# Kernel tuning notes

Measured on AMD Instinct MI355X. Metric: run time of the kernel, lower is better.

The kernel has to match this reference:

```python
import jax, jax.numpy as jnp
import numpy as np

B, S, D_IN, D = 2, 4096, 1024, 64  # batch, seq_len, input_dim, head dim d


def setup_inputs() -> dict:
    key = jax.random.key(0)
    k1, k2, k3, k4 = jax.random.split(key, 4)
    X = jax.random.normal(k1, (B, S, D_IN), dtype=jnp.float32)
    W_q = jax.random.normal(k2, (D_IN, 2 * D), dtype=jnp.float32) / np.sqrt(D_IN)
    W_k = jax.random.normal(k3, (D_IN, 2 * D), dtype=jnp.float32) / np.sqrt(D_IN)
    W_v = jax.random.normal(k4, (D_IN, 2 * D), dtype=jnp.float32) / np.sqrt(D_IN)
    lam = jnp.float32(0.8)
    return {"X": X, "W_q": W_q, "W_k": W_k, "W_v": W_v, "lam": lam}


def reference(X, W_q, W_k, W_v, lam):
    d = W_q.shape[-1] // 2
    Q = X @ W_q  # [B, S, 2d]
    K = X @ W_k  # [B, S, 2d]
    V = X @ W_v  # [B, S, 2d]
    Q1, Q2 = Q[..., :d], Q[..., d:]
    K1, K2 = K[..., :d], K[..., d:]
    s = 1.0 / jnp.sqrt(jnp.float32(d))
    A1 = jnp.einsum("bqd,bkd->bqk", Q1, K1) * s  # [B, S, S]
    A2 = jnp.einsum("bqd,bkd->bqk", Q2, K2) * s  # [B, S, S]
    P = jax.nn.softmax(A1, axis=-1) - lam * jax.nn.softmax(A2, axis=-1)
    return jnp.einsum("bqk,bkv->bqv", P, V)  # [B, S, 2d]
```

## Files before the change

kernel.cpp:

```cpp
#include <hip/hip_runtime.h>
#include <hip/hip_bf16.h>

typedef float f32x4 __attribute__((ext_vector_type(4)));
typedef float f32x16 __attribute__((ext_vector_type(16)));
typedef short bf16x8 __attribute__((ext_vector_type(8)));

#define MFMA16(A,B,C) __builtin_amdgcn_mfma_f32_16x16x32_bf16(A,B,C,0,0,0)
#define MFMA32(A,B,C) __builtin_amdgcn_mfma_f32_32x32x16_bf16(A,B,C,0,0,0)

__device__ __forceinline__ unsigned short f2bf(float f) {
    union { float f; unsigned u; } x; x.f = f;
    return (unsigned short)((x.u + 0x7FFFu + ((x.u >> 16) & 1u)) >> 16);
}

__device__ __forceinline__ float bf2f(unsigned short u) {
    union { unsigned u; float f; } x; x.u = ((unsigned)u) << 16; return x.f;
}

__device__ __forceinline__ unsigned fbits(float f) {
    union { float f; unsigned u; } x; x.f = f; return x.u;
}

__device__ __forceinline__ f32x16 zero16() {
    f32x16 z;
#pragma unroll
    for (int i = 0; i < 16; ++i) z[i] = 0.f;
    return z;
}

typedef const __attribute__((address_space(1))) unsigned int* as1_t;
typedef __attribute__((address_space(3))) unsigned int* as3_t;
__device__ __forceinline__ void gl_lds16(const unsigned short* g, unsigned short* l) {
    __builtin_amdgcn_global_load_lds((as1_t)g, (as3_t)l, 16, 0, 0);
}

__global__ void prep_wt(const float* __restrict__ Wq, const float* __restrict__ Wk,
                        const float* __restrict__ Wv, unsigned short* __restrict__ WT) {
    int w = blockIdx.x % 3;
    int kt = blockIdx.x / 3;
    const float* src = (w == 0) ? Wq : (w == 1) ? Wk : Wv;
    int k0 = kt * 32;
#pragma unroll
    for (int j = 0; j < 16; ++j) {
        int idx = threadIdx.x + j * 256;
        int r = idx >> 7, c = idx & 127;
        float v = src[(size_t)(k0 + r) * 128 + c];
        WT[(size_t)(w * 128 + c) * 1024 + k0 + r] = f2bf(v);
    }
}

__global__ __launch_bounds__(256) void prep_x(const float* __restrict__ X,
                                              unsigned short* __restrict__ Xb) {
    int i = blockIdx.x * 256 + threadIdx.x;
#pragma unroll
    for (int r = 0; r < 8; ++r) {
        int idx = i + r * 262144;
        float4 x = ((const float4*)X)[idx];
        ushort4 p;
        p.x = f2bf(x.x); p.y = f2bf(x.y); p.z = f2bf(x.z); p.w = f2bf(x.w);
        ((ushort4*)Xb)[idx] = p;
    }
}

__global__ __launch_bounds__(256) void proj(const unsigned short* __restrict__ Xb,
        const unsigned short* __restrict__ WT, unsigned short* __restrict__ Qc,
        unsigned short* __restrict__ Kc, unsigned short* __restrict__ VT) {
    int tid = threadIdx.x;
    int w = tid >> 6, lane = tid & 63;
    int lr = lane & 15, lg = lane >> 4;
    int wr = w >> 1, wc = w & 1;
    int m0 = blockIdx.x * 64;
    int n0 = blockIdx.y * 96;

    __shared__ __align__(16) unsigned short Ab[3][64 * 64];
    __shared__ __align__(16) unsigned short Bb[3][96 * 64];

    f32x4 acc[2][3];
#pragma unroll
    for (int i = 0; i < 2; ++i)
#pragma unroll
        for (int j = 0; j < 3; ++j) acc[i][j] = f32x4{0.f,0.f,0.f,0.f};

    int srow = lane >> 3;
    int sunit = lane & 7;
    const unsigned short* aSrc = Xb + (size_t)(m0 + srow) * 1024 + sunit * 8;
    const unsigned short* bSrc = WT + (size_t)(n0 + srow) * 1024 + sunit * 8;

    auto STAGE = [&](unsigned short* ad, unsigned short* bd, int st) {
        int kk = st * 64;
#pragma unroll
        for (int i = 0; i < 2; ++i) {
            int blk = w * 2 + i;
            gl_lds16(aSrc + (size_t)blk * 8 * 1024 + kk, ad + blk * 512);
        }
#pragma unroll
        for (int i = 0; i < 3; ++i) {
            int blk = w * 3 + i;
            gl_lds16(bSrc + (size_t)blk * 8 * 1024 + kk, bd + blk * 512);
        }
    };

    unsigned short *a0 = Ab[0], *a1 = Ab[1], *a2 = Ab[2];
    unsigned short *b0 = Bb[0], *b1 = Bb[1], *b2 = Bb[2];
    STAGE(a0, b0, 0);
    STAGE(a1, b1, 1);

    for (int st = 0; st < 16; ++st) {
        if (st < 15) asm volatile("s_waitcnt vmcnt(5)" ::: "memory");
        else         asm volatile("s_waitcnt vmcnt(0)" ::: "memory");
        __builtin_amdgcn_sched_barrier(0);
        __builtin_amdgcn_s_barrier();
        __builtin_amdgcn_sched_barrier(0);
        if (st + 2 < 16) STAGE(a2, b2, st + 2);

        const unsigned short* ab = a0;
        const unsigned short* bb = b0;
#pragma unroll
        for (int ksub = 0; ksub < 2; ++ksub) {
            int ko = ksub * 32 + lg * 8;
            bf16x8 af[2], bf[3];
#pragma unroll
            for (int mt = 0; mt < 2; ++mt)
                af[mt] = *(const bf16x8*)(ab + (wr * 32 + mt * 16 + lr) * 64 + ko);
#pragma unroll
            for (int nt = 0; nt < 3; ++nt)
                bf[nt] = *(const bf16x8*)(bb + (wc * 48 + nt * 16 + lr) * 64 + ko);
#pragma unroll
            for (int mt = 0; mt < 2; ++mt)
#pragma unroll
                for (int nt = 0; nt < 3; ++nt)
                    acc[mt][nt] = MFMA16(af[mt], bf[nt], acc[mt][nt]);
        }
        unsigned short* t;
        t = a0; a0 = a1; a1 = a2; a2 = t;
        t = b0; b0 = b1; b1 = b2; b2 = t;
    }

    int b = m0 >> 12;
    int sbase = (m0 & 4095) + wr * 32;
#pragma unroll
    for (int nt = 0; nt < 3; ++nt) {
        int gcol = n0 + wc * 48 + nt * 16 + lr;
        int tensor = gcol >> 7;
#pragma unroll
        for (int mt = 0; mt < 2; ++mt) {
            int sloc = sbase + mt * 16 + 4 * lg;
            if (tensor == 2) {
                int vcol = gcol & 127;
                int slocV = (sloc & ~15) | (((lg & 1) << 3) | ((lg >> 1) << 2));
                ushort4 pk;
                pk.x = f2bf(acc[mt][nt][0]); pk.y = f2bf(acc[mt][nt][1]);
                pk.z = f2bf(acc[mt][nt][2]); pk.w = f2bf(acc[mt][nt][3]);
                *(ushort4*)(VT + (size_t)(b * 128 + vcol) * 4096 + slocV) = pk;
            } else {
                int within = gcol & 127;
                int comp = within >> 6;
                int col64 = within & 63;
                float sc = (tensor == 0) ? 0.1803368801f : 1.0f;
                unsigned short* dst = (tensor == 0) ? Qc : Kc;
                size_t rowb = (size_t)(comp * 2 + b) * 4096 + sloc;
#pragma unroll
                for (int r = 0; r < 4; ++r)
                    dst[(rowb + r) * 64 + col64] = f2bf(acc[mt][nt][r] * sc);
            }
        }
    }
}

__global__ __launch_bounds__(256, 2) void attn(const unsigned short* __restrict__ Qc,
        const unsigned short* __restrict__ Kc, const unsigned short* __restrict__ VT,
        unsigned short* __restrict__ Opart, float* __restrict__ Lpart) {
    int tid = threadIdx.x;
    int wave = tid >> 6, lane = tid & 63;
    int l31 = lane & 31, hi = lane >> 5;
    int x7 = l31 & 7;
    int b = blockIdx.y;
    int comp = blockIdx.z >> 2, split = blockIdx.z & 3;
    int q0 = blockIdx.x * 128 + wave * 32;
    int kstart = split * 1024;

    __shared__ __align__(16) unsigned short kb3[3][64 * 64];
    __shared__ __align__(16) unsigned short vb3[3][128 * 64];

    const unsigned short* Qp = Qc + ((size_t)(comp * 2 + b) * 4096 + q0 + l31) * 64 + hi * 8;
    bf16x8 qB0 = *(const bf16x8*)(Qp);
    bf16x8 qB1 = *(const bf16x8*)(Qp + 16);
    bf16x8 qB2 = *(const bf16x8*)(Qp + 32);
    bf16x8 qB3 = *(const bf16x8*)(Qp + 48);

    f32x16 o[4];
#pragma unroll
    for (int i = 0; i < 4; ++i) o[i] = zero16();
    f32x16 ol = zero16();
    bf16x8 ones;
#pragma unroll
    for (int i = 0; i < 8; ++i) ones[i] = (short)0x3F80;

    const unsigned short* kSrc = Kc + ((size_t)(comp * 2 + b) * 4096 + kstart
                                       + wave * 8 + (lane >> 3)) * 64
                                    + ((lane & 7) ^ (lane >> 3)) * 8;
    const unsigned short* vSrc = VT + ((size_t)b * 128 + (tid >> 3)) * 4096
                                    + kstart + ((lane & 7) ^ (lane >> 3)) * 8;

    auto STAGE = [&](unsigned short* kd, unsigned short* vd, int it) {
        const unsigned short* ks = kSrc + (size_t)it * 4096;
        gl_lds16(ks,        kd + wave * 512);
        gl_lds16(ks + 2048, kd + 2048 + wave * 512);
        const unsigned short* vs = vSrc + it * 64;
#pragma unroll
        for (int ri = 0; ri < 4; ++ri)
            gl_lds16(vs + (size_t)ri * 32 * 4096, vd + ri * 2048 + wave * 512);
    };

    unsigned short *k0 = kb3[0], *k1 = kb3[1], *k2 = kb3[2];
    unsigned short *v0 = vb3[0], *v1 = vb3[1], *v2 = vb3[2];
    STAGE(k0, v0, 0);
    STAGE(k1, v1, 1);

    for (int it = 0; it < 16; ++it) {
        if (it < 15) asm volatile("s_waitcnt vmcnt(6)" ::: "memory");
        else         asm volatile("s_waitcnt vmcnt(0)" ::: "memory");
        __builtin_amdgcn_sched_barrier(0);
        __builtin_amdgcn_s_barrier();
        __builtin_amdgcn_sched_barrier(0);
        if (it + 2 < 16) STAGE(k2, v2, it + 2);

        const unsigned short* kb = k0;
        const unsigned short* vb = v0;

        f32x16 st0 = zero16(), st1 = zero16();
        __builtin_amdgcn_s_setprio(1);
#pragma unroll
        for (int j = 0; j < 4; ++j) {
            int ku = ((j * 2 + hi) ^ x7) * 8;
            bf16x8 kA0 = *(const bf16x8*)(kb + l31 * 64 + ku);
            bf16x8 kA1 = *(const bf16x8*)(kb + (32 + l31) * 64 + ku);
            bf16x8 qj = (j == 0) ? qB0 : (j == 1) ? qB1 : (j == 2) ? qB2 : qB3;
            st0 = MFMA32(kA0, qj, st0);
            st1 = MFMA32(kA1, qj, st1);
        }
        __builtin_amdgcn_s_setprio(0);

        union W4 { unsigned u[4]; bf16x8 v; };
        W4 wA0, wB0, wA1, wB1;
#pragma unroll
        for (int i2 = 0; i2 < 4; ++i2) {
            float a0 = __builtin_amdgcn_exp2f(st0[2 * i2]);
            float a1 = __builtin_amdgcn_exp2f(st0[2 * i2 + 1]);
            float a2 = __builtin_amdgcn_exp2f(st0[8 + 2 * i2]);
            float a3 = __builtin_amdgcn_exp2f(st0[9 + 2 * i2]);
            float b0 = __builtin_amdgcn_exp2f(st1[2 * i2]);
            float b1 = __builtin_amdgcn_exp2f(st1[2 * i2 + 1]);
            float b2 = __builtin_amdgcn_exp2f(st1[8 + 2 * i2]);
            float b3 = __builtin_amdgcn_exp2f(st1[9 + 2 * i2]);
            wA0.u[i2] = __builtin_amdgcn_perm(fbits(a1), fbits(a0), 0x07060302);
            wB0.u[i2] = __builtin_amdgcn_perm(fbits(a3), fbits(a2), 0x07060302);
            wA1.u[i2] = __builtin_amdgcn_perm(fbits(b1), fbits(b0), 0x07060302);
            wB1.u[i2] = __builtin_amdgcn_perm(fbits(b3), fbits(b2), 0x07060302);
        }

        __builtin_amdgcn_s_setprio(1);
        ol = MFMA32(wA0.v, ones, ol);
        ol = MFMA32(wB0.v, ones, ol);
        ol = MFMA32(wA1.v, ones, ol);
        ol = MFMA32(wB1.v, ones, ol);
#pragma unroll
        for (int vt = 0; vt < 4; ++vt) {
            const unsigned short* vrow = vb + (vt * 32 + l31) * 64;
            o[vt] = MFMA32(wA0.v, *(const bf16x8*)(vrow + ((0 + hi) ^ x7) * 8), o[vt]);
            o[vt] = MFMA32(wB0.v, *(const bf16x8*)(vrow + ((2 + hi) ^ x7) * 8), o[vt]);
            o[vt] = MFMA32(wA1.v, *(const bf16x8*)(vrow + ((4 + hi) ^ x7) * 8), o[vt]);
            o[vt] = MFMA32(wB1.v, *(const bf16x8*)(vrow + ((6 + hi) ^ x7) * 8), o[vt]);
        }
        __builtin_amdgcn_s_setprio(0);

        unsigned short* t;
        t = k0; k0 = k1; k1 = k2; k2 = t;
        t = v0; v0 = v1; v1 = v2; v2 = t;
    }

    int base = (b * 2 + comp) * 4 + split;
    unsigned short* op = Opart + (size_t)base * 4096 * 128;
#pragma unroll
    for (int vt = 0; vt < 4; ++vt)
#pragma unroll
        for (int r = 0; r < 16; ++r) {
            int qr = (r & 3) + 8 * (r >> 2) + 4 * hi;
            op[(size_t)(q0 + qr) * 128 + vt * 32 + l31] = f2bf(o[vt][r]);
        }
    if (l31 == 0) {
        float* lp = Lpart + (size_t)base * 4096 + q0;
#pragma unroll
        for (int r = 0; r < 16; ++r)
            lp[(r & 3) + 8 * (r >> 2) + 4 * hi] = ol[r];
    }
}

__global__ __launch_bounds__(256) void combine(const unsigned short* __restrict__ Opart,
        const float* __restrict__ Lpart, const float* __restrict__ lamp,
        float* __restrict__ out) {
    float lam = lamp[0];
    int i = blockIdx.x * 256 + threadIdx.x;
    int row = i >> 5;
    int c4  = i & 31;
    int b = row >> 12, q = row & 4095;

    float l1 = 0.f, l2 = 0.f;
#pragma unroll
    for (int s = 0; s < 4; ++s) {
        l1 += Lpart[((size_t)((b * 2 + 0) * 4 + s)) * 4096 + q];
        l2 += Lpart[((size_t)((b * 2 + 1) * 4 + s)) * 4096 + q];
    }
    float rl1 = 1.0f / l1, rl2 = 1.0f / l2;

    size_t qoff = (size_t)q * 128 + c4 * 4;
    float a0 = 0.f, a1 = 0.f, a2 = 0.f, a3 = 0.f;
    float c0 = 0.f, c1 = 0.f, c2 = 0.f, c3 = 0.f;
#pragma unroll
    for (int s = 0; s < 4; ++s) {
        ushort4 p1 = *(const ushort4*)(Opart + (size_t)((b * 2 + 0) * 4 + s) * 4096 * 128 + qoff);
        ushort4 p2 = *(const ushort4*)(Opart + (size_t)((b * 2 + 1) * 4 + s) * 4096 * 128 + qoff);
        a0 += bf2f(p1.x); a1 += bf2f(p1.y); a2 += bf2f(p1.z); a3 += bf2f(p1.w);
        c0 += bf2f(p2.x); c1 += bf2f(p2.y); c2 += bf2f(p2.z); c3 += bf2f(p2.w);
    }
    float4 r;
    r.x = a0 * rl1 - lam * c0 * rl2;
    r.y = a1 * rl1 - lam * c1 * rl2;
    r.z = a2 * rl1 - lam * c2 * rl2;
    r.w = a3 * rl1 - lam * c3 * rl2;
    ((float4*)out)[i] = r;
}

extern "C" void kernel_launch(void* const* d_in, const int* in_sizes, int n_in,
                              void* d_out, int out_size, void* d_ws, size_t ws_size,
                              hipStream_t stream) {
    const float* X   = (const float*)d_in[0];
    const float* Wq  = (const float*)d_in[1];
    const float* Wk  = (const float*)d_in[2];
    const float* Wv  = (const float*)d_in[3];
    const float* lam = (const float*)d_in[4];
    float* out = (float*)d_out;

    char* ws = (char*)d_ws;
    unsigned short* Qc = (unsigned short*)(ws);
    unsigned short* Kc = (unsigned short*)(ws + 2097152);
    unsigned short* VT = (unsigned short*)(ws + 4194304);
    unsigned short* WT = (unsigned short*)(ws + 6291456);
    unsigned short* Xb = (unsigned short*)(ws + 7077888);
    unsigned short* Opart = (unsigned short*)(ws + 6291456);
    float* Lpart = (float*)(ws + 23068672);

    prep_wt<<<dim3(96), dim3(256), 0, stream>>>(Wq, Wk, Wv, WT);
    prep_x<<<dim3(1024), dim3(256), 0, stream>>>(X, Xb);
    proj<<<dim3(128, 4), dim3(256), 0, stream>>>(Xb, WT, Qc, Kc, VT);
    attn<<<dim3(32, 2, 8), dim3(256), 0, stream>>>(Qc, Kc, VT, Opart, Lpart);
    combine<<<dim3(1024), dim3(256), 0, stream>>>(Opart, Lpart, lam, out);
}
```

Measured before the change: 75.33 us.

## Split attention keys eight ways with double buffering and scalar row-sum accumulation

Doubles the key-split count for attention from 4 to 8, so twice as many blocks run with half the key range each. The LDS ring shrinks from triple to double buffering to allow three blocks per CU, with an extra barrier per iteration. Row sums of the softmax numerator are now accumulated in fp32 scalar adds plus a cross-lane shuffle, replacing the MFMA-with-ones trick. The intent is better occupancy and a shorter critical path per block, at the cost of twice the partial-output traffic and reads in the combine kernel.

Result: slower. 80.35 us (+6.7%).

```diff
diff --git a/kernel.cpp b/kernel.cpp
--- a/kernel.cpp
+++ b/kernel.cpp
@@ -167,7 +167,7 @@
     }
 }
 
-__global__ __launch_bounds__(256, 2) void attn(const unsigned short* __restrict__ Qc,
+__global__ __launch_bounds__(256, 3) void attn(const unsigned short* __restrict__ Qc,
         const unsigned short* __restrict__ Kc, const unsigned short* __restrict__ VT,
         unsigned short* __restrict__ Opart, float* __restrict__ Lpart) {
     int tid = threadIdx.x;
@@ -175,12 +175,12 @@
     int l31 = lane & 31, hi = lane >> 5;
     int x7 = l31 & 7;
     int b = blockIdx.y;
-    int comp = blockIdx.z >> 2, split = blockIdx.z & 3;
+    int comp = blockIdx.z >> 3, split = blockIdx.z & 7;
     int q0 = blockIdx.x * 128 + wave * 32;
-    int kstart = split * 1024;
-
-    __shared__ __align__(16) unsigned short kb3[3][64 * 64];
-    __shared__ __align__(16) unsigned short vb3[3][128 * 64];
+    int kstart = split * 512;
+
+    __shared__ __align__(16) unsigned short kb2[2][64 * 64];
+    __shared__ __align__(16) unsigned short vb2[2][128 * 64];
 
     const unsigned short* Qp = Qc + ((size_t)(comp * 2 + b) * 4096 + q0 + l31) * 64 + hi * 8;
     bf16x8 qB0 = *(const bf16x8*)(Qp);
@@ -191,10 +191,7 @@
     f32x16 o[4];
 #pragma unroll
     for (int i = 0; i < 4; ++i) o[i] = zero16();
-    f32x16 ol = zero16();
-    bf16x8 ones;
-#pragma unroll
-    for (int i = 0; i < 8; ++i) ones[i] = (short)0x3F80;
+    float lsum = 0.f;
 
     const unsigned short* kSrc = Kc + ((size_t)(comp * 2 + b) * 4096 + kstart
                                        + wave * 8 + (lane >> 3)) * 64
@@ -212,18 +209,17 @@
             gl_lds16(vs + (size_t)ri * 32 * 4096, vd + ri * 2048 + wave * 512);
     };
 
-    unsigned short *k0 = kb3[0], *k1 = kb3[1], *k2 = kb3[2];
-    unsigned short *v0 = vb3[0], *v1 = vb3[1], *v2 = vb3[2];
+    unsigned short *k0 = kb2[0], *k1 = kb2[1];
+    unsigned short *v0 = vb2[0], *v1 = vb2[1];
     STAGE(k0, v0, 0);
-    STAGE(k1, v1, 1);
-
-    for (int it = 0; it < 16; ++it) {
-        if (it < 15) asm volatile("s_waitcnt vmcnt(6)" ::: "memory");
-        else         asm volatile("s_waitcnt vmcnt(0)" ::: "memory");
+
+    for (int it = 0; it < 8; ++it) {
+        if (it + 1 < 8) STAGE(k1, v1, it + 1);
+        if (it + 1 < 8) asm volatile("s_waitcnt vmcnt(6)" ::: "memory");
+        else            asm volatile("s_waitcnt vmcnt(0)" ::: "memory");
         __builtin_amdgcn_sched_barrier(0);
         __builtin_amdgcn_s_barrier();
         __builtin_amdgcn_sched_barrier(0);
-        if (it + 2 < 16) STAGE(k2, v2, it + 2);
 
         const unsigned short* kb = k0;
         const unsigned short* vb = v0;
@@ -253,6 +249,7 @@
             float b1 = __builtin_amdgcn_exp2f(st1[2 * i2 + 1]);
             float b2 = __builtin_amdgcn_exp2f(st1[8 + 2 * i2]);
             float b3 = __builtin_amdgcn_exp2f(st1[9 + 2 * i2]);
+            lsum += (a0 + a1) + (a2 + a3) + (b0 + b1) + (b2 + b3);
             wA0.u[i2] = __builtin_amdgcn_perm(fbits(a1), fbits(a0), 0x07060302);
             wB0.u[i2] = __builtin_amdgcn_perm(fbits(a3), fbits(a2), 0x07060302);
             wA1.u[i2] = __builtin_amdgcn_perm(fbits(b1), fbits(b0), 0x07060302);
@@ -260,10 +257,6 @@
         }
 
         __builtin_amdgcn_s_setprio(1);
-        ol = MFMA32(wA0.v, ones, ol);
-        ol = MFMA32(wB0.v, ones, ol);
-        ol = MFMA32(wA1.v, ones, ol);
-        ol = MFMA32(wB1.v, ones, ol);
 #pragma unroll
         for (int vt = 0; vt < 4; ++vt) {
             const unsigned short* vrow = vb + (vt * 32 + l31) * 64;
@@ -274,12 +267,14 @@
         }
         __builtin_amdgcn_s_setprio(0);
 
+        if (it + 1 < 8) __builtin_amdgcn_s_barrier();
+
         unsigned short* t;
-        t = k0; k0 = k1; k1 = k2; k2 = t;
-        t = v0; v0 = v1; v1 = v2; v2 = t;
-    }
-
-    int base = (b * 2 + comp) * 4 + split;
+        t = k0; k0 = k1; k1 = t;
+        t = v0; v0 = v1; v1 = t;
+    }
+
+    int base = (b * 2 + comp) * 8 + split;
     unsigned short* op = Opart + (size_t)base * 4096 * 128;
 #pragma unroll
     for (int vt = 0; vt < 4; ++vt)
@@ -288,12 +283,9 @@
             int qr = (r & 3) + 8 * (r >> 2) + 4 * hi;
             op[(size_t)(q0 + qr) * 128 + vt * 32 + l31] = f2bf(o[vt][r]);
         }
-    if (l31 == 0) {
-        float* lp = Lpart + (size_t)base * 4096 + q0;
-#pragma unroll
-        for (int r = 0; r < 16; ++r)
-            lp[(r & 3) + 8 * (r >> 2) + 4 * hi] = ol[r];
-    }
+    float ls = lsum + __shfl_xor(lsum, 32, 64);
+    if (hi == 0)
+        Lpart[(size_t)base * 4096 + q0 + l31] = ls;
 }
 
 __global__ __launch_bounds__(256) void combine(const unsigned short* __restrict__ Opart,
@@ -307,9 +299,9 @@
 
     float l1 = 0.f, l2 = 0.f;
 #pragma unroll
-    for (int s = 0; s < 4; ++s) {
-        l1 += Lpart[((size_t)((b * 2 + 0) * 4 + s)) * 4096 + q];
-        l2 += Lpart[((size_t)((b * 2 + 1) * 4 + s)) * 4096 + q];
+    for (int s = 0; s < 8; ++s) {
+        l1 += Lpart[((size_t)((b * 2 + 0) * 8 + s)) * 4096 + q];
+        l2 += Lpart[((size_t)((b * 2 + 1) * 8 + s)) * 4096 + q];
     }
     float rl1 = 1.0f / l1, rl2 = 1.0f / l2;
 
@@ -317,9 +309,9 @@
     float a0 = 0.f, a1 = 0.f, a2 = 0.f, a3 = 0.f;
     float c0 = 0.f, c1 = 0.f, c2 = 0.f, c3 = 0.f;
 #pragma unroll
-    for (int s = 0; s < 4; ++s) {
-        ushort4 p1 = *(const ushort4*)(Opart + (size_t)((b * 2 + 0) * 4 + s) * 4096 * 128 + qoff);
-        ushort4 p2 = *(const ushort4*)(Opart + (size_t)((b * 2 + 1) * 4 + s) * 4096 * 128 + qoff);
+    for (int s = 0; s < 8; ++s) {
+        ushort4 p1 = *(const ushort4*)(Opart + (size_t)((b * 2 + 0) * 8 + s) * 4096 * 128 + qoff);
+        ushort4 p2 = *(const ushort4*)(Opart + (size_t)((b * 2 + 1) * 8 + s) * 4096 * 128 + qoff);
         a0 += bf2f(p1.x); a1 += bf2f(p1.y); a2 += bf2f(p1.z); a3 += bf2f(p1.w);
         c0 += bf2f(p2.x); c1 += bf2f(p2.y); c2 += bf2f(p2.z); c3 += bf2f(p2.w);
     }
@@ -348,11 +340,11 @@
     unsigned short* WT = (unsigned short*)(ws + 6291456);
     unsigned short* Xb = (unsigned short*)(ws + 7077888);
     unsigned short* Opart = (unsigned short*)(ws + 6291456);
-    float* Lpart = (float*)(ws + 23068672);
+    float* Lpart = (float*)(ws + 39845888);
 
     prep_wt<<<dim3(96), dim3(256), 0, stream>>>(Wq, Wk, Wv, WT);
     prep_x<<<dim3(1024), dim3(256), 0, stream>>>(X, Xb);
     proj<<<dim3(128, 4), dim3(256), 0, stream>>>(Xb, WT, Qc, Kc, VT);
-    attn<<<dim3(32, 2, 8), dim3(256), 0, stream>>>(Qc, Kc, VT, Opart, Lpart);
+    attn<<<dim3(32, 2, 16), dim3(256), 0, stream>>>(Qc, Kc, VT, Opart, Lpart);
     combine<<<dim3(1024), dim3(256), 0, stream>>>(Opart, Lpart, lam, out);
 }
```

## Merge prep kernels and compute softmax row sums with VALU adds

Applied to the files above, without the earlier changes.

Combines the weight-transpose and X-to-bf16 conversion kernels into one launch that dispatches on block index, removing one kernel launch and its gap. In the attention kernel, the per-row sum of exponentials is now accumulated in fp32 scalar adds and reduced with a cross-half shuffle, replacing four extra MFMA-by-ones instructions per tile. This frees matrix-core issue slots but adds VALU work, and the sum now uses unrounded fp32 values rather than the bf16-rounded weights fed to the PV product.

Measured after the change: 70.59 us. -6.3%, faster.

```diff
diff --git a/kernel.cpp b/kernel.cpp
--- a/kernel.cpp
+++ b/kernel.cpp
@@ -34,31 +34,32 @@
     __builtin_amdgcn_global_load_lds((as1_t)g, (as3_t)l, 16, 0, 0);
 }
 
-__global__ void prep_wt(const float* __restrict__ Wq, const float* __restrict__ Wk,
-                        const float* __restrict__ Wv, unsigned short* __restrict__ WT) {
-    int w = blockIdx.x % 3;
-    int kt = blockIdx.x / 3;
-    const float* src = (w == 0) ? Wq : (w == 1) ? Wk : Wv;
-    int k0 = kt * 32;
-#pragma unroll
-    for (int j = 0; j < 16; ++j) {
-        int idx = threadIdx.x + j * 256;
-        int r = idx >> 7, c = idx & 127;
-        float v = src[(size_t)(k0 + r) * 128 + c];
-        WT[(size_t)(w * 128 + c) * 1024 + k0 + r] = f2bf(v);
-    }
-}
-
-__global__ __launch_bounds__(256) void prep_x(const float* __restrict__ X,
-                                              unsigned short* __restrict__ Xb) {
-    int i = blockIdx.x * 256 + threadIdx.x;
-#pragma unroll
-    for (int r = 0; r < 8; ++r) {
-        int idx = i + r * 262144;
-        float4 x = ((const float4*)X)[idx];
-        ushort4 p;
-        p.x = f2bf(x.x); p.y = f2bf(x.y); p.z = f2bf(x.z); p.w = f2bf(x.w);
-        ((ushort4*)Xb)[idx] = p;
+__global__ __launch_bounds__(256) void prep(const float* __restrict__ Wq,
+        const float* __restrict__ Wk, const float* __restrict__ Wv,
+        const float* __restrict__ X, unsigned short* __restrict__ WT,
+        unsigned short* __restrict__ Xb) {
+    if (blockIdx.x < 96) {
+        int w = blockIdx.x % 3;
+        int kt = blockIdx.x / 3;
+        const float* src = (w == 0) ? Wq : (w == 1) ? Wk : Wv;
+        int k0 = kt * 32;
+#pragma unroll
+        for (int j = 0; j < 16; ++j) {
+            int idx = threadIdx.x + j * 256;
+            int r = idx >> 7, c = idx & 127;
+            float v = src[(size_t)(k0 + r) * 128 + c];
+            WT[(size_t)(w * 128 + c) * 1024 + k0 + r] = f2bf(v);
+        }
+    } else {
+        int i = (blockIdx.x - 96) * 256 + threadIdx.x;
+#pragma unroll
+        for (int r = 0; r < 8; ++r) {
+            int idx = i + r * 262144;
+            float4 x = ((const float4*)X)[idx];
+            ushort4 p;
+            p.x = f2bf(x.x); p.y = f2bf(x.y); p.z = f2bf(x.z); p.w = f2bf(x.w);
+            ((ushort4*)Xb)[idx] = p;
+        }
     }
 }
 
@@ -191,10 +192,7 @@
     f32x16 o[4];
 #pragma unroll
     for (int i = 0; i < 4; ++i) o[i] = zero16();
-    f32x16 ol = zero16();
-    bf16x8 ones;
-#pragma unroll
-    for (int i = 0; i < 8; ++i) ones[i] = (short)0x3F80;
+    float lsum = 0.f;
 
     const unsigned short* kSrc = Kc + ((size_t)(comp * 2 + b) * 4096 + kstart
                                        + wave * 8 + (lane >> 3)) * 64
@@ -253,6 +251,7 @@
             float b1 = __builtin_amdgcn_exp2f(st1[2 * i2 + 1]);
             float b2 = __builtin_amdgcn_exp2f(st1[8 + 2 * i2]);
             float b3 = __builtin_amdgcn_exp2f(st1[9 + 2 * i2]);
+            lsum += (a0 + a1) + (a2 + a3) + (b0 + b1) + (b2 + b3);
             wA0.u[i2] = __builtin_amdgcn_perm(fbits(a1), fbits(a0), 0x07060302);
             wB0.u[i2] = __builtin_amdgcn_perm(fbits(a3), fbits(a2), 0x07060302);
             wA1.u[i2] = __builtin_amdgcn_perm(fbits(b1), fbits(b0), 0x07060302);
@@ -260,10 +259,6 @@
         }
 
         __builtin_amdgcn_s_setprio(1);
-        ol = MFMA32(wA0.v, ones, ol);
-        ol = MFMA32(wB0.v, ones, ol);
-        ol = MFMA32(wA1.v, ones, ol);
-        ol = MFMA32(wB1.v, ones, ol);
 #pragma unroll
         for (int vt = 0; vt < 4; ++vt) {
             const unsigned short* vrow = vb + (vt * 32 + l31) * 64;
@@ -288,12 +283,9 @@
             int qr = (r & 3) + 8 * (r >> 2) + 4 * hi;
             op[(size_t)(q0 + qr) * 128 + vt * 32 + l31] = f2bf(o[vt][r]);
         }
-    if (l31 == 0) {
-        float* lp = Lpart + (size_t)base * 4096 + q0;
-#pragma unroll
-        for (int r = 0; r < 16; ++r)
-            lp[(r & 3) + 8 * (r >> 2) + 4 * hi] = ol[r];
-    }
+    float ls = lsum + __shfl_xor(lsum, 32, 64);
+    if (hi == 0)
+        Lpart[(size_t)base * 4096 + q0 + l31] = ls;
 }
 
 __global__ __launch_bounds__(256) void combine(const unsigned short* __restrict__ Opart,
@@ -350,8 +342,7 @@
     unsigned short* Opart = (unsigned short*)(ws + 6291456);
     float* Lpart = (float*)(ws + 23068672);
 
-    prep_wt<<<dim3(96), dim3(256), 0, stream>>>(Wq, Wk, Wv, WT);
-    prep_x<<<dim3(1024), dim3(256), 0, stream>>>(X, Xb);
+    prep<<<dim3(1120), dim3(256), 0, stream>>>(Wq, Wk, Wv, X, WT, Xb);
     proj<<<dim3(128, 4), dim3(256), 0, stream>>>(Xb, WT, Qc, Kc, VT);
     attn<<<dim3(32, 2, 8), dim3(256), 0, stream>>>(Qc, Kc, VT, Opart, Lpart);
     combine<<<dim3(1024), dim3(256), 0, stream>>>(Opart, Lpart, lam, out);
```
